# Optimization experiments

Measured on AMD Instinct MI355X. Metric: run time of the kernel, lower is better.

The kernel has to match this reference:

```python
import jax, jax.numpy as jnp
import numpy as np

SEQ_LEN, BATCH, INPUT, HIDDEN, OUTPUT = 2048, 64, 256, 256, 256


def setup_inputs() -> dict:
    key = jax.random.key(0)
    ks = jax.random.split(key, 6)
    return {
        "x": jax.random.normal(ks[0], (SEQ_LEN, BATCH, INPUT), dtype=jnp.float32),
        "h0": jax.random.normal(ks[1], (BATCH, HIDDEN), dtype=jnp.float32),
        "i2h_weight": jax.random.normal(ks[2], (INPUT + HIDDEN, HIDDEN), dtype=jnp.float32) * 0.05,
        "i2h_bias": jax.random.normal(ks[3], (HIDDEN,), dtype=jnp.float32) * 0.05,
        "h2o_weight": jax.random.normal(ks[4], (HIDDEN, OUTPUT), dtype=jnp.float32) * 0.05,
        "h2o_bias": jax.random.normal(ks[5], (OUTPUT,), dtype=jnp.float32) * 0.05,
    }


def reference(x, h0, i2h_weight, i2h_bias, h2o_weight, h2o_bias):
    # Vanilla RNN: per timestep t:
    #   h = tanh(concat(x_t, h) @ W_i2h + b_i2h)
    #   y_t = h @ W_h2o + b_h2o
    # Split W_i2h into input/hidden blocks so the concat is expressed as two GEMMs.
    w_xh = i2h_weight[:x.shape[-1]]   # [input, hidden]
    w_hh = i2h_weight[x.shape[-1]:]   # [hidden, hidden]

    def step(h, x_t):
        h_new = jnp.tanh(x_t @ w_xh + h @ w_hh + i2h_bias)  # [batch, hidden]
        y_t = h_new @ h2o_weight + h2o_bias                  # [batch, output]
        return h_new, y_t

    _, outputs = jax.lax.scan(step, h0, x)  # outputs: [seq, batch, output]
    return outputs
```

## Files before the change

### kernel.cpp

```cpp
#include <hip/hip_runtime.h>
#include <cstdint>
#include <cstddef>

typedef __attribute__((ext_vector_type(8))) short short8;
typedef __attribute__((ext_vector_type(4))) float f32x4;
typedef __attribute__((ext_vector_type(2))) float f32x2;
typedef __attribute__((ext_vector_type(2))) unsigned int u32x2;

#define SEQ 2048
#define NB  64
#define HID 256
#define M_TOTAL (SEQ*NB)

__device__ __forceinline__ unsigned short f2bf(float x){
  unsigned u = __float_as_uint(x);
  u += 0x7fffu + ((u>>16)&1u);
  return (unsigned short)(u>>16);
}

__global__ void k_convert_x(const float* __restrict__ x, unsigned short* __restrict__ xb){
  size_t i = (size_t)blockIdx.x*256 + threadIdx.x;
  f32x4 v = ((const f32x4*)x)[i];
  unsigned a0=f2bf(v[0]), a1=f2bf(v[1]), a2=f2bf(v[2]), a3=f2bf(v[3]);
  u32x2 o; o[0] = a0 | (a1<<16); o[1] = a2 | (a3<<16);
  ((u32x2*)xb)[i] = o;
}

__global__ void k_convert_w(const float* __restrict__ i2h, const float* __restrict__ h2o,
                            unsigned short* __restrict__ BT1, unsigned short* __restrict__ BT3){
  int k = blockIdx.x; int n = threadIdx.x;
  BT1[n*256+k] = f2bf(i2h[k*256+n]);
  BT3[n*256+k] = f2bf(h2o[k*256+n]);
}

__global__ __launch_bounds__(256) void k_gemm(
    const unsigned short* __restrict__ A, const unsigned short* __restrict__ BT,
    const float* __restrict__ bias, float* __restrict__ C)
{
  __shared__ __align__(16) unsigned short As[128*64];
  __shared__ __align__(16) unsigned short Bs[128*64];
  int tid = threadIdx.x;
  int bm = blockIdx.x, bn = blockIdx.y;
  int l = tid & 63, wv = tid >> 6;
  int wm = wv >> 1, wn = wv & 1;
  int lr = l & 15, lq = l >> 4;

  f32x4 acc[4][4];
  #pragma unroll
  for (int i=0;i<4;i++)
    #pragma unroll
    for (int j=0;j<4;j++) acc[i][j] = (f32x4)0.f;

  for (int kb=0; kb<4; ++kb){
    int k0 = kb*64;
    #pragma unroll
    for (int it=0; it<4; ++it){
      int f = it*256 + tid;
      int m = f >> 3;
      int kk = (f & 7) * 8;
      short8 va = *(const short8*)(A  + (size_t)(bm*128+m)*256 + k0 + kk);
      short8 vb = *(const short8*)(BT + (size_t)(bn*128+m)*256 + k0 + kk);
      *(short8*)(As + m*64 + kk) = va;
      *(short8*)(Bs + m*64 + kk) = vb;
    }
    __syncthreads();
    #pragma unroll
    for (int kt=0; kt<2; ++kt){
      short8 af[4], bfr[4];
      #pragma unroll
      for (int mt=0;mt<4;mt++){
        int row = wm*64 + mt*16 + lr;
        af[mt] = *(const short8*)(As + row*64 + kt*32 + lq*8);
      }
      #pragma unroll
      for (int nt=0;nt<4;nt++){
        int row = wn*64 + nt*16 + lr;
        bfr[nt] = *(const short8*)(Bs + row*64 + kt*32 + lq*8);
      }
      #pragma unroll
      for (int mt=0;mt<4;mt++)
        #pragma unroll
        for (int nt=0;nt<4;nt++)
          acc[mt][nt] = __builtin_amdgcn_mfma_f32_16x16x32_bf16(af[mt], bfr[nt], acc[mt][nt], 0, 0, 0);
    }
    __syncthreads();
  }
  #pragma unroll
  for (int nt=0;nt<4;nt++){
    int gn = bn*128 + wn*64 + nt*16 + lr;
    float bv = bias[gn];
    #pragma unroll
    for (int mt=0;mt<4;mt++){
      int gm = bm*128 + wm*64 + mt*16 + lq*4;
      #pragma unroll
      for (int r=0;r<4;r++)
        C[(size_t)(gm+r)*256 + gn] = acc[mt][nt][r] + bv;
    }
  }
}

__global__ __launch_bounds__(1024, 4) void k_scan(
    const float* __restrict__ i2h,
    const float* __restrict__ h0,
    const float* __restrict__ pre,
    unsigned short* __restrict__ H)
{
  __shared__ float hbuf[256];
  __shared__ float red[3*256];
  int b   = blockIdx.x;
  int tid = threadIdx.x;
  int kc  = tid >> 8;
  int j   = tid & 255;

  f32x2 w2[32];
  const float* Wp = i2h + (size_t)(256 + kc*64)*256 + j;
  #pragma unroll
  for (int i=0;i<32;i++){
    w2[i][0] = Wp[(size_t)(2*i  )*256];
    w2[i][1] = Wp[(size_t)(2*i+1)*256];
  }
  if (tid < 256) hbuf[tid] = h0[b*256 + tid];
  __syncthreads();

  bool lead = (kc == 0);
  float pv = lead ? pre[(size_t)b*256 + j] : 0.f;

  for (int t=0; t<SEQ; ++t){
    float pn = 0.f;
    if (lead && t+1 < SEQ) pn = pre[((size_t)(t+1)*NB + b)*256 + j];

    const f32x2* hp = (const f32x2*)(hbuf + kc*64);
    f32x2 a2 = (f32x2)0.f;
    #pragma unroll
    for (int i=0;i<32;i++){
      f32x2 h2 = hp[i];
      a2 += w2[i]*h2;
    }
    float acc = a2[0] + a2[1];

    if (!lead) red[(kc-1)*256 + j] = acc;
    __syncthreads();
    if (lead){
      float s = acc + red[j] + red[256+j] + red[512+j] + pv;
      float e = __expf(2.f*s);
      float h = 1.f - 2.f/(e+1.f);
      hbuf[j] = h;
      H[((size_t)t*NB + b)*256 + j] = f2bf(h);
      pv = pn;
    }
    __syncthreads();
  }
}

extern "C" void kernel_launch(void* const* d_in, const int* in_sizes, int n_in,
                              void* d_out, int out_size, void* d_ws, size_t ws_size,
                              hipStream_t stream) {
  const float* x     = (const float*)d_in[0];
  const float* h0    = (const float*)d_in[1];
  const float* i2h   = (const float*)d_in[2];
  const float* i2h_b = (const float*)d_in[3];
  const float* h2o   = (const float*)d_in[4];
  const float* h2o_b = (const float*)d_in[5];
  float* out = (float*)d_out;

  unsigned short* xb  = (unsigned short*)d_ws;
  unsigned short* BT1 = (unsigned short*)((char*)d_ws + (size_t)M_TOTAL*HID*2);
  unsigned short* BT3 = BT1 + 256*256;

  k_convert_x<<<M_TOTAL*HID/(256*4), 256, 0, stream>>>(x, xb);
  k_convert_w<<<256, 256, 0, stream>>>(i2h, h2o, BT1, BT3);

  dim3 g1(M_TOTAL/128, 2);
  k_gemm<<<g1, 256, 0, stream>>>(xb, BT1, i2h_b, out);
  k_scan<<<NB, 1024, 0, stream>>>(i2h, h0, out, xb);
  k_gemm<<<g1, 256, 0, stream>>>(xb, BT3, h2o_b, out);
}
```

Baseline: 1.823 ms.

## Repartition recurrent matvec into 16 k-chunks with vec4 outputs per thread

```diff
diff --git a/kernel.cpp b/kernel.cpp
--- a/kernel.cpp
+++ b/kernel.cpp
@@ -105,48 +105,54 @@
     const float* __restrict__ pre,
     unsigned short* __restrict__ H)
 {
-  __shared__ float hbuf[256];
-  __shared__ float red[3*256];
+  __shared__ __align__(16) float hbuf[256];
+  __shared__ __align__(16) float red[16*256];
   int b   = blockIdx.x;
   int tid = threadIdx.x;
-  int kc  = tid >> 8;
-  int j   = tid & 255;
+  int jg  = tid & 63;
+  int kc  = tid >> 6;
 
-  f32x2 w2[32];
-  const float* Wp = i2h + (size_t)(256 + kc*64)*256 + j;
+  f32x4 w[16];
+  const float* Wp = i2h + (size_t)(256 + kc*16)*256 + jg*4;
   #pragma unroll
-  for (int i=0;i<32;i++){
-    w2[i][0] = Wp[(size_t)(2*i  )*256];
-    w2[i][1] = Wp[(size_t)(2*i+1)*256];
+  for (int i=0;i<16;i++)
+    w[i] = *(const f32x4*)(Wp + (size_t)i*256);
+
+  if (tid < 256) hbuf[tid] = h0[b*256 + tid];
+
+  float pv = 0.f, p1 = 0.f;
+  if (tid < 256){
+    pv = pre[(size_t)b*256 + tid];
+    p1 = pre[((size_t)1*NB + b)*256 + tid];
   }
-  if (tid < 256) hbuf[tid] = h0[b*256 + tid];
   __syncthreads();
 
-  bool lead = (kc == 0);
-  float pv = lead ? pre[(size_t)b*256 + j] : 0.f;
+  float* myred = red + kc*256 + jg*4;
 
   for (int t=0; t<SEQ; ++t){
-    float pn = 0.f;
-    if (lead && t+1 < SEQ) pn = pre[((size_t)(t+1)*NB + b)*256 + j];
+    const f32x4* hp = (const f32x4*)(hbuf + kc*16);
+    f32x4 acc = (f32x4)0.f;
+    #pragma unroll
+    for (int i=0;i<4;i++){
+      f32x4 h4 = hp[i];
+      acc += h4[0]*w[4*i+0];
+      acc += h4[1]*w[4*i+1];
+      acc += h4[2]*w[4*i+2];
+      acc += h4[3]*w[4*i+3];
+    }
+    *(f32x4*)myred = acc;
+    __syncthreads();
 
-    const f32x2* hp = (const f32x2*)(hbuf + kc*64);
-    f32x2 a2 = (f32x2)0.f;
-    #pragma unroll
-    for (int i=0;i<32;i++){
-      f32x2 h2 = hp[i];
-      a2 += w2[i]*h2;
-    }
-    float acc = a2[0] + a2[1];
-
-    if (!lead) red[(kc-1)*256 + j] = acc;
-    __syncthreads();
-    if (lead){
-      float s = acc + red[j] + red[256+j] + red[512+j] + pv;
+    if (tid < 256){
+      float p2 = (t+2 < SEQ) ? pre[((size_t)(t+2)*NB + b)*256 + tid] : 0.f;
+      float s = pv;
+      #pragma unroll
+      for (int k2=0;k2<16;k2++) s += red[k2*256 + tid];
       float e = __expf(2.f*s);
       float h = 1.f - 2.f/(e+1.f);
-      hbuf[j] = h;
-      H[((size_t)t*NB + b)*256 + j] = f2bf(h);
-      pv = pn;
+      hbuf[tid] = h;
+      H[((size_t)t*NB + b)*256 + tid] = f2bf(h);
+      pv = p1; p1 = p2;
     }
     __syncthreads();
   }
```

Result: faster. 1.653 ms (-9.3%).

## Drop second barrier in RNN scan via redundant per-wave tanh and double-buffered reduction

Applied to the files above, without the earlier changes.

```diff
diff --git a/kernel.cpp b/kernel.cpp
--- a/kernel.cpp
+++ b/kernel.cpp
@@ -105,12 +105,16 @@
     const float* __restrict__ pre,
     unsigned short* __restrict__ H)
 {
-  __shared__ float hbuf[256];
-  __shared__ float red[3*256];
-  int b   = blockIdx.x;
-  int tid = threadIdx.x;
-  int kc  = tid >> 8;
-  int j   = tid & 255;
+  __shared__ __align__(16) float hbuf[16][64];
+  __shared__ __align__(16) float red[2][4][256];
+  int b    = blockIdx.x;
+  int tid  = threadIdx.x;
+  int lane = tid & 63;
+  int w    = tid >> 6;
+  int jq   = w & 3;
+  int kc   = w >> 2;
+  int j    = jq*64 + lane;
+  int jh   = kc*64 + lane;
 
   f32x2 w2[32];
   const float* Wp = i2h + (size_t)(256 + kc*64)*256 + j;
@@ -119,36 +123,38 @@
     w2[i][0] = Wp[(size_t)(2*i  )*256];
     w2[i][1] = Wp[(size_t)(2*i+1)*256];
   }
-  if (tid < 256) hbuf[tid] = h0[b*256 + tid];
-  __syncthreads();
 
-  bool lead = (kc == 0);
-  float pv = lead ? pre[(size_t)b*256 + j] : 0.f;
+  hbuf[w][lane] = h0[b*256 + jh];
+
+  float pv = pre[(size_t)b*256 + jh];
+  float p1 = pre[((size_t)1*NB + b)*256 + jh];
+
+  const float* hb = hbuf[w];
 
   for (int t=0; t<SEQ; ++t){
-    float pn = 0.f;
-    if (lead && t+1 < SEQ) pn = pre[((size_t)(t+1)*NB + b)*256 + j];
+    f32x2 a0 = (f32x2)0.f, a1 = (f32x2)0.f;
+    const f32x4* hp = (const f32x4*)hb;
+    #pragma unroll
+    for (int i=0;i<16;i++){
+      f32x4 h4 = hp[i];
+      f32x2 hlo = __builtin_shufflevector(h4, h4, 0, 1);
+      f32x2 hhi = __builtin_shufflevector(h4, h4, 2, 3);
+      asm("v_pk_fma_f32 %0, %1, %2, %0" : "+v"(a0) : "v"(w2[2*i  ]), "v"(hlo));
+      asm("v_pk_fma_f32 %0, %1, %2, %0" : "+v"(a1) : "v"(w2[2*i+1]), "v"(hhi));
+    }
+    f32x2 a = a0 + a1;
+    red[t&1][kc][j] = a[0] + a[1];
+    __syncthreads();
 
-    const f32x2* hp = (const f32x2*)(hbuf + kc*64);
-    f32x2 a2 = (f32x2)0.f;
-    #pragma unroll
-    for (int i=0;i<32;i++){
-      f32x2 h2 = hp[i];
-      a2 += w2[i]*h2;
-    }
-    float acc = a2[0] + a2[1];
-
-    if (!lead) red[(kc-1)*256 + j] = acc;
-    __syncthreads();
-    if (lead){
-      float s = acc + red[j] + red[256+j] + red[512+j] + pv;
-      float e = __expf(2.f*s);
-      float h = 1.f - 2.f/(e+1.f);
-      hbuf[j] = h;
-      H[((size_t)t*NB + b)*256 + j] = f2bf(h);
-      pv = pn;
-    }
-    __syncthreads();
+    float p2 = (t+2 < SEQ) ? pre[((size_t)(t+2)*NB + b)*256 + jh] : 0.f;
+    const float* rd = &red[t&1][0][jh];
+    float s = pv + rd[0] + rd[256] + rd[512] + rd[768];
+    float e = __expf(2.f*s);
+    float h = 1.f - 2.f/(e+1.f);
+    hbuf[w][lane] = h;
+    if (jq == 0)
+      H[((size_t)t*NB + b)*256 + jh] = f2bf(h);
+    pv = p1; p1 = p2;
   }
 }
 
```

Result: slower. 1.965 ms (+7.8%).
